# Optimization experiments

Measured on AMD Instinct MI355X. Metric: run time of the kernel, lower is better.

Reference implementation:

```python
import jax, jax.numpy as jnp
import numpy as np

NUM_HEADS = 8  # from init_kwargs
SR = 2         # sr_ratio from init_kwargs


def layernorm(t, g, b, eps=1e-5):
    mu = jnp.mean(t, axis=-1, keepdims=True)
    var = jnp.mean((t - mu) ** 2, axis=-1, keepdims=True)
    return (t - mu) * jax.lax.rsqrt(var + eps) * g + b


def setup_inputs() -> dict:
    key = jax.random.key(0)
    ks = jax.random.split(key, 6)
    B, C = 4, 256
    Hx = Wx = 64
    Hz = Wz = 32
    N = Hz * Wz + Hx * Wx  # 5120 (template tokens first, then search tokens)
    s = 0.02
    return {
        "x": jax.random.normal(ks[0], (B, N, C), jnp.float32),
        "Wq": jax.random.normal(ks[1], (C, C), jnp.float32) * s,          # nn.Linear(dim, dim, bias=False)
        "Wkv": jax.random.normal(ks[2], (2 * C, C), jnp.float32) * s,     # nn.Linear(dim, 2*dim, bias=False)
        "Wsr": jax.random.normal(ks[3], (C, C, SR, SR), jnp.float32) * s, # Conv2d(dim, dim, k=sr, stride=sr) OIHW
        "bsr": jnp.zeros((C,), jnp.float32),
        "gamma": jnp.ones((C,), jnp.float32),
        "beta": jnp.zeros((C,), jnp.float32),
        "Wproj": jax.random.normal(ks[4], (C, C), jnp.float32) * s,
        "bproj": jnp.zeros((C,), jnp.float32),
        "H_x": Hx, "W_x": Wx, "H_z": Hz, "W_z": Wz,
    }


def reference(x, Wq, Wkv, Wsr, bsr, gamma, beta, Wproj, bproj, H_x, W_x, H_z, W_z):
    B, N, C = x.shape
    h = NUM_HEADS
    d = C // h
    scale = d ** -0.5
    Nz, Nx = H_z * W_z, H_x * W_x

    # q for all tokens: [B, h, N, d]
    q = (x @ Wq.T).reshape(B, N, h, d).transpose(0, 2, 1, 3)

    # spatial reduction (sr_ratio > 1 branch): strided conv + layernorm on each stream
    z_tok, x_tok = x[:, :Nz], x[:, Nz:]
    ker = jnp.transpose(Wsr, (2, 3, 1, 0))  # OIHW -> HWIO

    def sr_branch(t, H, W):
        img = t.reshape(B, H, W, C)  # NHWC; same layout as torch NCHW reshape
        out = jax.lax.conv_general_dilated(
            img, ker, window_strides=(SR, SR), padding="VALID",
            dimension_numbers=("NHWC", "HWIO", "NHWC")) + bsr
        out = out.reshape(B, -1, C)
        return layernorm(out, gamma, beta)

    x_ = sr_branch(x_tok, H_x, W_x)  # [B, (Hx/sr)*(Wx/sr), C]
    z_ = sr_branch(z_tok, H_z, W_z)  # [B, (Hz/sr)*(Wz/sr), C]
    zL = z_.shape[1]
    cat = jnp.concatenate([z_, x_], axis=1)  # [B, L, C]

    kv = (cat @ Wkv.T).reshape(B, -1, 2, h, d).transpose(2, 0, 3, 1, 4)  # [2, B, h, L, d]
    k, v = kv[0], kv[1]

    q_z, q_x = q[:, :, :Nz], q[:, :, Nz:]
    k_z, v_z = k[:, :, :zL], v[:, :, :zL]

    # template queries attend only to reduced template keys/values
    attn_z = jax.nn.softmax(jnp.einsum("bhqd,bhkd->bhqk", q_z, k_z) * scale, axis=-1)
    out_z = jnp.einsum("bhqk,bhkd->bhqd", attn_z, v_z).transpose(0, 2, 1, 3).reshape(B, Nz, C)

    # search queries attend to full (template+search) reduced keys/values
    attn_x = jax.nn.softmax(jnp.einsum("bhqd,bhkd->bhqk", q_x, k) * scale, axis=-1)
    out_x = jnp.einsum("bhqk,bhkd->bhqd", attn_x, v).transpose(0, 2, 1, 3).reshape(B, Nx, C)

    out = jnp.concatenate([out_z, out_x], axis=1)
    return out @ Wproj.T + bproj
```

## Files before the change

kernel.cpp:

```cpp
#include <hip/hip_runtime.h>
#include <hip/hip_bf16.h>
#include <cstddef>

#define BATCH 4
#define CCH 256
#define NHEAD 8
#define DHEAD 32
#define NZ 1024
#define NX 4096
#define NTOK 5120
#define LKV 1280
#define QC 0.25503486f

typedef __attribute__((ext_vector_type(8))) short bf16x8;
typedef __attribute__((ext_vector_type(4))) float floatx4;

__device__ inline short f2bf(float f) {
  __hip_bfloat16 h = __float2bfloat16(f);
  return __builtin_bit_cast(short, h);
}
__device__ inline unsigned int pk2(float a, float b) {
  unsigned int lo = (unsigned short)f2bf(a);
  unsigned int hi = (unsigned short)f2bf(b);
  return lo | (hi << 16);
}
__device__ inline unsigned int cvtpk(float a, float b) {
  unsigned int r;
  asm("v_cvt_pk_bf16_f32 %0, %1, %2" : "=v"(r) : "v"(a), "v"(b));
  return r;
}
__device__ inline void cvt8(const float* __restrict__ src, short* __restrict__ dst, int i) {
  float4 v0 = ((const float4*)src)[i * 2];
  float4 v1 = ((const float4*)src)[i * 2 + 1];
  uint4 u;
  u.x = pk2(v0.x, v0.y); u.y = pk2(v0.z, v0.w);
  u.z = pk2(v1.x, v1.y); u.w = pk2(v1.z, v1.w);
  ((uint4*)dst)[i] = u;
}

__global__ __launch_bounds__(256) void prep_weights(const float* __restrict__ Wq,
                                                    const float* __restrict__ Wkv,
                                                    const float* __restrict__ Wproj,
                                                    const float* __restrict__ Wsr,
                                                    const float* __restrict__ x,
                                                    short* __restrict__ Wqb,
                                                    short* __restrict__ Wkvb,
                                                    short* __restrict__ Wprojb,
                                                    short* __restrict__ Wkb,
                                                    short* __restrict__ xb) {
  int blk = blockIdx.x, tid = threadIdx.x;
  if (blk < 32) {
    cvt8(Wq, Wqb, blk * 256 + tid);
  } else if (blk < 96) {
    cvt8(Wkv, Wkvb, (blk - 32) * 256 + tid);
  } else if (blk < 128) {
    cvt8(Wproj, Wprojb, (blk - 96) * 256 + tid);
  } else if (blk < 1152) {
    int i = (blk - 128) * 256 + tid;
    int co = i >> 10;
    int rem = i & 1023;
    int di = rem >> 9, dj = (rem >> 8) & 1, ci = rem & 255;
    Wkb[i] = f2bf(Wsr[((co * 256 + ci) * 2 + di) * 2 + dj]);
  } else {
    cvt8(x, xb, (blk - 1152) * 256 + tid);
  }
}

#define G64_DECL()                                                           \
  __shared__ short As[64][72];                                               \
  __shared__ short Bs[64][72];                                               \
  int tid = threadIdx.x;                                                     \
  int wave = tid >> 6, lg = (tid & 63) >> 4, lr = tid & 15;                  \
  int sr = tid >> 2, sc = tid & 3;                                           \
  floatx4 acc[4] = {{0.f,0.f,0.f,0.f},{0.f,0.f,0.f,0.f},                     \
                    {0.f,0.f,0.f,0.f},{0.f,0.f,0.f,0.f}};

#define G64_MFMA8()                                                          \
    __syncthreads();                                                         \
    {                                                                        \
      bf16x8 af0 = *(bf16x8*)&As[wave * 16 + lr][lg * 8];                    \
      bf16x8 af1 = *(bf16x8*)&As[wave * 16 + lr][32 + lg * 8];               \
      _Pragma("unroll") for (int n = 0; n < 4; ++n) {                        \
        bf16x8 bf0 = *(bf16x8*)&Bs[n * 16 + lr][lg * 8];                     \
        bf16x8 bf1 = *(bf16x8*)&Bs[n * 16 + lr][32 + lg * 8];                \
        acc[n] = __builtin_amdgcn_mfma_f32_16x16x32_bf16(af0, bf0, acc[n], 0, 0, 0); \
        acc[n] = __builtin_amdgcn_mfma_f32_16x16x32_bf16(af1, bf1, acc[n], 0, 0, 0); \
      }                                                                      \
    }

__global__ __launch_bounds__(256) void gemm_qconv(const short* __restrict__ xb,
                                                  const short* __restrict__ Wqb,
                                                  const short* __restrict__ Wkb,
                                                  short* __restrict__ qbf,
                                                  float* __restrict__ cat_pre) {
  G64_DECL()
  int bidx = blockIdx.x;
  if (bidx < 1280) {
    int bm = (bidx >> 2) * 64, bn = (bidx & 3) * 64;
    for (int k0 = 0; k0 < 256; k0 += 64) {
      bf16x8 a0 = *(const bf16x8*)&xb[(size_t)(bm + sr) * 256 + k0 + sc * 8];
      bf16x8 a1 = *(const bf16x8*)&xb[(size_t)(bm + sr) * 256 + k0 + (sc + 4) * 8];
      bf16x8 b0 = *(const bf16x8*)&Wqb[(size_t)(bn + sr) * 256 + k0 + sc * 8];
      bf16x8 b1 = *(const bf16x8*)&Wqb[(size_t)(bn + sr) * 256 + k0 + (sc + 4) * 8];
      __syncthreads();
      *(bf16x8*)&As[sr][sc * 8] = a0;
      *(bf16x8*)&As[sr][(sc + 4) * 8] = a1;
      *(bf16x8*)&Bs[sr][sc * 8] = b0;
      *(bf16x8*)&Bs[sr][(sc + 4) * 8] = b1;
      G64_MFMA8()
    }
#pragma unroll
    for (int n = 0; n < 4; ++n) {
      int c = bn + 16 * n + lr;
      int h = c >> 5, d = c & 31;
#pragma unroll
      for (int reg = 0; reg < 4; ++reg) {
        int m = bm + wave * 16 + 4 * lg + reg;
        int b = m / NTOK, tok = m - b * NTOK;
        qbf[((size_t)(b * 8 + h) * NTOK + tok) * 32 + d] = f2bf(acc[n][reg] * QC);
      }
    }
  } else {
    int idx = bidx - 1280;
    int mt = idx >> 2;
    int bm = mt * 64, bn = (idx & 3) * 64;
    int bq = mt / 20;
    int tloc = (mt % 20) * 64 + sr;
    for (int k0 = 0; k0 < 1024; k0 += 64) {
      int di = k0 >> 9, dj = (k0 >> 8) & 1;
      int srow;
      if (tloc < 256) {
        int oi = tloc >> 4, oj = tloc & 15;
        srow = bq * NTOK + (2 * oi + di) * 32 + (2 * oj + dj);
      } else {
        int tt = tloc - 256;
        int oi = tt >> 5, oj = tt & 31;
        srow = bq * NTOK + NZ + (2 * oi + di) * 64 + (2 * oj + dj);
      }
      int cb = k0 & 255;
      bf16x8 a0 = *(const bf16x8*)&xb[(size_t)srow * 256 + cb + sc * 8];
      bf16x8 a1 = *(const bf16x8*)&xb[(size_t)srow * 256 + cb + (sc + 4) * 8];
      bf16x8 b0 = *(const bf16x8*)&Wkb[(size_t)(bn + sr) * 1024 + k0 + sc * 8];
      bf16x8 b1 = *(const bf16x8*)&Wkb[(size_t)(bn + sr) * 1024 + k0 + (sc + 4) * 8];
      __syncthreads();
      *(bf16x8*)&As[sr][sc * 8] = a0;
      *(bf16x8*)&As[sr][(sc + 4) * 8] = a1;
      *(bf16x8*)&Bs[sr][sc * 8] = b0;
      *(bf16x8*)&Bs[sr][(sc + 4) * 8] = b1;
      G64_MFMA8()
    }
#pragma unroll
    for (int n = 0; n < 4; ++n) {
      int c = bn + 16 * n + lr;
#pragma unroll
      for (int reg = 0; reg < 4; ++reg) {
        int m = bm + wave * 16 + 4 * lg + reg;
        cat_pre[(size_t)m * 256 + c] = acc[n][reg];
      }
    }
  }
}

__global__ __launch_bounds__(256) void gemm_kv64(const short* __restrict__ A,
                                                 const short* __restrict__ Bm,
                                                 short* __restrict__ Kbf,
                                                 short* __restrict__ Vtb) {
  G64_DECL()
  int bm = blockIdx.y * 64, bn = blockIdx.x * 64;
  for (int k0 = 0; k0 < 256; k0 += 64) {
    bf16x8 a0 = *(const bf16x8*)&A[(size_t)(bm + sr) * 256 + k0 + sc * 8];
    bf16x8 a1 = *(const bf16x8*)&A[(size_t)(bm + sr) * 256 + k0 + (sc + 4) * 8];
    bf16x8 b0 = *(const bf16x8*)&Bm[(size_t)(bn + sr) * 256 + k0 + sc * 8];
    bf16x8 b1 = *(const bf16x8*)&Bm[(size_t)(bn + sr) * 256 + k0 + (sc + 4) * 8];
    __syncthreads();
    *(bf16x8*)&As[sr][sc * 8] = a0;
    *(bf16x8*)&As[sr][(sc + 4) * 8] = a1;
    *(bf16x8*)&Bs[sr][sc * 8] = b0;
    *(bf16x8*)&Bs[sr][(sc + 4) * 8] = b1;
    G64_MFMA8()
  }
#pragma unroll
  for (int n = 0; n < 4; ++n) {
    int c = bn + 16 * n + lr;
#pragma unroll
    for (int reg = 0; reg < 4; ++reg) {
      int m = bm + wave * 16 + 4 * lg + reg;
      int b = m / LKV, kvg = m - b * LKV;
      if (c < 256) {
        int h = c >> 5, d = c & 31;
        Kbf[((size_t)(b * 8 + h) * LKV + kvg) * 32 + d] = f2bf(acc[n][reg]);
      } else {
        int cc = c - 256;
        int h = cc >> 5, d = cc & 31;
        int tile = kvg >> 6, kvin = kvg & 63;
        Vtb[(((size_t)(b * 8 + h) * 20 + tile) * 32 + d) * 64 + kvin] = f2bf(acc[n][reg]);
      }
    }
  }
}

__global__ __launch_bounds__(256) void gemm_proj64(const short* __restrict__ A,
                                                   const short* __restrict__ Bm,
                                                   const float* __restrict__ bias,
                                                   float* __restrict__ Cm) {
  G64_DECL()
  int bm = blockIdx.y * 64, bn = blockIdx.x * 64;
  for (int k0 = 0; k0 < 256; k0 += 64) {
    bf16x8 a0 = *(const bf16x8*)&A[(size_t)(bm + sr) * 256 + k0 + sc * 8];
    bf16x8 a1 = *(const bf16x8*)&A[(size_t)(bm + sr) * 256 + k0 + (sc + 4) * 8];
    bf16x8 b0 = *(const bf16x8*)&Bm[(size_t)(bn + sr) * 256 + k0 + sc * 8];
    bf16x8 b1 = *(const bf16x8*)&Bm[(size_t)(bn + sr) * 256 + k0 + (sc + 4) * 8];
    __syncthreads();
    *(bf16x8*)&As[sr][sc * 8] = a0;
    *(bf16x8*)&As[sr][(sc + 4) * 8] = a1;
    *(bf16x8*)&Bs[sr][sc * 8] = b0;
    *(bf16x8*)&Bs[sr][(sc + 4) * 8] = b1;
    G64_MFMA8()
  }
#pragma unroll
  for (int n = 0; n < 4; ++n) {
    int c = bn + 16 * n + lr;
    float bv = bias[c];
#pragma unroll
    for (int reg = 0; reg < 4; ++reg) {
      int m = bm + wave * 16 + 4 * lg + reg;
      Cm[(size_t)m * 256 + c] = acc[n][reg] + bv;
    }
  }
}

__global__ __launch_bounds__(256) void ln_kernel(const float* __restrict__ cat_pre,
                                                 const float* __restrict__ bsr,
                                                 const float* __restrict__ gamma,
                                                 const float* __restrict__ beta,
                                                 short* __restrict__ catb) {
  int row = blockIdx.x * 4 + (threadIdx.x >> 6);
  int lane = threadIdx.x & 63;
  float4 v = *(const float4*)&cat_pre[(size_t)row * 256 + lane * 4];
  float4 bb = *(const float4*)&bsr[lane * 4];
  v.x += bb.x; v.y += bb.y; v.z += bb.z; v.w += bb.w;
  float s = (v.x + v.y) + (v.z + v.w);
#pragma unroll
  for (int mask = 1; mask < 64; mask <<= 1) s += __shfl_xor(s, mask, 64);
  float mu = s * (1.f / 256.f);
  float4 dv;
  dv.x = v.x - mu; dv.y = v.y - mu; dv.z = v.z - mu; dv.w = v.w - mu;
  float q = dv.x * dv.x + dv.y * dv.y + dv.z * dv.z + dv.w * dv.w;
#pragma unroll
  for (int mask = 1; mask < 64; mask <<= 1) q += __shfl_xor(q, mask, 64);
  float rs = rsqrtf(q * (1.f / 256.f) + 1e-5f);
  float4 g = *(const float4*)&gamma[lane * 4];
  float4 be = *(const float4*)&beta[lane * 4];
  uint2 st;
  st.x = pk2(dv.x * rs * g.x + be.x, dv.y * rs * g.y + be.y);
  st.y = pk2(dv.z * rs * g.z + be.z, dv.w * rs * g.w + be.w);
  *(uint2*)&catb[(size_t)row * 256 + lane * 4] = st;
}

__global__ __launch_bounds__(64) void attn_fused(const short* __restrict__ qbf,
                                                 const short* __restrict__ Kbf,
                                                 const short* __restrict__ Vtb,
                                                 short* __restrict__ attn_out) {
  int orig = blockIdx.x;
  int xcd = orig & 7, s = orig >> 3;
  int bh, q0, kvlen;
  if (s < 256) {
    bh = xcd + 8 * (s >> 6);
    q0 = NZ + (s & 63) * 64;
    kvlen = LKV;
  } else {
    int s2 = s - 256;
    bh = xcd + 8 * (s2 >> 4);
    q0 = (s2 & 15) * 64;
    kvlen = 256;
  }
  int b = bh >> 3, hh = bh & 7;
  int tid = threadIdx.x;
  int lane = tid & 63, lg = lane >> 4, lr = lane & 15;

  __shared__ short Ps[64][72];

  int qtok = q0;
  const short* qb = qbf + ((size_t)bh * NTOK + qtok) * 32;
  bf16x8 qf[4];
#pragma unroll
  for (int qi = 0; qi < 4; ++qi)
    qf[qi] = *(const bf16x8*)&qb[(16 * qi + lr) * 32 + lg * 8];

  const short* Kb = Kbf + (size_t)bh * LKV * 32;
  const short* Vb = Vtb + (size_t)bh * 20 * 2048;

  const short onebf = (short)0x3F80;
  bf16x8 onesb = {onebf, onebf, onebf, onebf, onebf, onebf, onebf, onebf};

  floatx4 oacc[4][2];
  floatx4 lacc[4];
#pragma unroll
  for (int qi = 0; qi < 4; ++qi) {
    lacc[qi] = (floatx4){0.f, 0.f, 0.f, 0.f};
#pragma unroll
    for (int n = 0; n < 2; ++n) oacc[qi][n] = (floatx4){0.f, 0.f, 0.f, 0.f};
  }

  bf16x8 kfc[4], vfc[2][2];
#pragma unroll
  for (int m = 0; m < 4; ++m)
    kfc[m] = *(const bf16x8*)&Kb[(size_t)(16 * m + lr) * 32 + lg * 8];
#pragma unroll
  for (int n = 0; n < 2; ++n)
#pragma unroll
    for (int kb = 0; kb < 2; ++kb)
      vfc[n][kb] = *(const bf16x8*)&Vb[(16 * n + lr) * 64 + kb * 32 + lg * 8];

  for (int l0 = 0; l0 < kvlen; l0 += 64) {
    __builtin_amdgcn_sched_barrier(0);
#pragma unroll
    for (int qi = 0; qi < 4; ++qi) {
      floatx4 st[4];
#pragma unroll
      for (int m = 0; m < 4; ++m)
        st[m] = __builtin_amdgcn_mfma_f32_16x16x32_bf16(
            kfc[m], qf[qi], (floatx4){0.f, 0.f, 0.f, 0.f}, 0, 0, 0);
      int pr = 16 * qi + lr;
#pragma unroll
      for (int m = 0; m < 4; ++m) {
        float p0 = __builtin_amdgcn_exp2f(st[m][0]);
        float p1 = __builtin_amdgcn_exp2f(st[m][1]);
        float p2 = __builtin_amdgcn_exp2f(st[m][2]);
        float p3 = __builtin_amdgcn_exp2f(st[m][3]);
        uint2 w;
        w.x = cvtpk(p0, p1);
        w.y = cvtpk(p2, p3);
        *(uint2*)&Ps[pr][16 * m + 4 * lg] = w;
      }
    }

    bf16x8 kfn[4], vfn[2][2];
    int l1 = l0 + 64;
    if (l1 < kvlen) {
      const short* Vbt = Vb + (l1 >> 6) * 2048;
#pragma unroll
      for (int m = 0; m < 4; ++m)
        kfn[m] = *(const bf16x8*)&Kb[(size_t)(l1 + 16 * m + lr) * 32 + lg * 8];
#pragma unroll
      for (int n = 0; n < 2; ++n)
#pragma unroll
        for (int kb = 0; kb < 2; ++kb)
          vfn[n][kb] = *(const bf16x8*)&Vbt[(16 * n + lr) * 64 + kb * 32 + lg * 8];
    }

    __builtin_amdgcn_sched_barrier(0);

#pragma unroll
    for (int qi = 0; qi < 4; ++qi)
#pragma unroll
      for (int kb = 0; kb < 2; ++kb) {
        bf16x8 pf = *(bf16x8*)&Ps[16 * qi + lr][kb * 32 + lg * 8];
#pragma unroll
        for (int n = 0; n < 2; ++n)
          oacc[qi][n] = __builtin_amdgcn_mfma_f32_16x16x32_bf16(pf, vfc[n][kb], oacc[qi][n], 0, 0, 0);
        lacc[qi] = __builtin_amdgcn_mfma_f32_16x16x32_bf16(pf, onesb, lacc[qi], 0, 0, 0);
      }

#pragma unroll
    for (int m = 0; m < 4; ++m) kfc[m] = kfn[m];
#pragma unroll
    for (int n = 0; n < 2; ++n)
#pragma unroll
      for (int kb = 0; kb < 2; ++kb) vfc[n][kb] = vfn[n][kb];
  }

#pragma unroll
  for (int qi = 0; qi < 4; ++qi)
#pragma unroll
    for (int reg = 0; reg < 4; ++reg) {
      float inv = 1.f / lacc[qi][reg];
      int gr = b * NTOK + qtok + 16 * qi + 4 * lg + reg;
      short* ob = attn_out + (size_t)gr * CCH + hh * DHEAD;
      ob[lr]      = f2bf(oacc[qi][0][reg] * inv);
      ob[16 + lr] = f2bf(oacc[qi][1][reg] * inv);
    }
}

extern "C" void kernel_launch(void* const* d_in, const int* in_sizes, int n_in,
                              void* d_out, int out_size, void* d_ws, size_t ws_size,
                              hipStream_t stream) {
  (void)in_sizes; (void)n_in; (void)out_size; (void)ws_size;
  const float* x     = (const float*)d_in[0];
  const float* Wq    = (const float*)d_in[1];
  const float* Wkv   = (const float*)d_in[2];
  const float* Wsr   = (const float*)d_in[3];
  const float* bsr   = (const float*)d_in[4];
  const float* gamma = (const float*)d_in[5];
  const float* beta  = (const float*)d_in[6];
  const float* Wproj = (const float*)d_in[7];
  const float* bproj = (const float*)d_in[8];
  float* out = (float*)d_out;
  float* ws  = (float*)d_ws;

  short* qbf      = (short*)ws;
  short* attn_out = (short*)(ws + 2621440);
  float* cat_pre  = ws + 7864320;
  short* catb     = (short*)(ws + 9175040);
  short* Kbf      = (short*)(ws + 9830400);
  short* Vtb      = (short*)(ws + 10485760);
  short* Wqb      = (short*)(ws + 11141120);
  short* Wkvb     = (short*)(ws + 11173888);
  short* Wkb      = (short*)(ws + 11239424);
  short* Wprojb   = (short*)(ws + 11370496);
  short* xb       = attn_out;

  prep_weights<<<3712, 256, 0, stream>>>(Wq, Wkv, Wproj, Wsr, x, Wqb, Wkvb, Wprojb, Wkb, xb);
  gemm_qconv<<<1600, 256, 0, stream>>>(xb, Wqb, Wkb, qbf, cat_pre);
  ln_kernel<<<1280, 256, 0, stream>>>(cat_pre, bsr, gamma, beta, catb);
  gemm_kv64<<<dim3(8, 80), 256, 0, stream>>>(catb, Wkvb, Kbf, Vtb);
  attn_fused<<<2560, 64, 0, stream>>>(qbf, Kbf, Vtb, attn_out);
  gemm_proj64<<<dim3(4, 320), 256, 0, stream>>>(attn_out, Wprojb, bproj, out);
}
```

Measured before the change: 191.2 us.

## Double-buffer P tiles in attention, compute row sums on VALU, cheaper bf16 pack

Restructures the attention inner loop into a software pipeline with two shared-memory P buffers. The QK^T and exp for tile t+1 now overlap with the PV MFMAs for tile t, and the sched barriers are removed. The row-sum MFMA against a ones vector is replaced by per-lane float accumulation plus shuffle reductions, which cuts MFMA work by a third in the PV phase. The inline cvt_pk bf16 instruction is replaced by a round-half-up bit trick using v_perm. The new pack differs slightly in rounding, and the row sum now uses the unrounded fp32 P, so it no longer matches the bf16 P that feeds the PV MFMAs.

```diff
diff --git a/kernel.cpp b/kernel.cpp
--- a/kernel.cpp
+++ b/kernel.cpp
@@ -24,10 +24,10 @@
   unsigned int hi = (unsigned short)f2bf(b);
   return lo | (hi << 16);
 }
-__device__ inline unsigned int cvtpk(float a, float b) {
-  unsigned int r;
-  asm("v_cvt_pk_bf16_f32 %0, %1, %2" : "=v"(r) : "v"(a), "v"(b));
-  return r;
+__device__ inline unsigned int pk2f(float a, float b) {
+  unsigned int ua = __builtin_bit_cast(unsigned int, a) + 0x8000u;
+  unsigned int ub = __builtin_bit_cast(unsigned int, b) + 0x8000u;
+  return __builtin_amdgcn_perm(ub, ua, 0x07060302u);
 }
 __device__ inline void cvt8(const float* __restrict__ src, short* __restrict__ dst, int i) {
   float4 v0 = ((const float4*)src)[i * 2];
@@ -257,6 +257,45 @@
   *(uint2*)&catb[(size_t)row * 256 + lane * 4] = st;
 }
 
+#define ATTN_HALF(RD, WR, T, LOADK)                                             \
+  {                                                                             \
+    const short* Vbt = Vb + ((T) + 1) * 2048;                                   \
+    _Pragma("unroll") for (int n = 0; n < 2; ++n)                               \
+      _Pragma("unroll") for (int kb = 0; kb < 2; ++kb)                          \
+        vfn[n][kb] = *(const bf16x8*)&Vbt[(16 * n + lr) * 64 + kb * 32 + lg * 8]; \
+    if (LOADK) {                                                                \
+      _Pragma("unroll") for (int m = 0; m < 4; ++m)                             \
+        kfn[m] = *(const bf16x8*)&Kb[(size_t)(((T) + 2) * 64 + 16 * m + lr) * 32 + lg * 8]; \
+    }                                                                           \
+    _Pragma("unroll") for (int qi = 0; qi < 4; ++qi) {                          \
+      floatx4 st[4];                                                            \
+      _Pragma("unroll") for (int m = 0; m < 4; ++m)                             \
+        st[m] = __builtin_amdgcn_mfma_f32_16x16x32_bf16(                        \
+            kfc[m], qf[qi], (floatx4){0.f, 0.f, 0.f, 0.f}, 0, 0, 0);            \
+      int pr = 16 * qi + lr;                                                    \
+      _Pragma("unroll") for (int m = 0; m < 4; ++m) {                           \
+        float p0 = __builtin_amdgcn_exp2f(st[m][0]);                            \
+        float p1 = __builtin_amdgcn_exp2f(st[m][1]);                            \
+        float p2 = __builtin_amdgcn_exp2f(st[m][2]);                            \
+        float p3 = __builtin_amdgcn_exp2f(st[m][3]);                            \
+        lsum[qi] += (p0 + p1) + (p2 + p3);                                      \
+        uint2 w;                                                                \
+        w.x = pk2f(p0, p1);                                                     \
+        w.y = pk2f(p2, p3);                                                     \
+        *(uint2*)&WR[pr][16 * m + 4 * lg] = w;                                  \
+      }                                                                         \
+    }                                                                           \
+    _Pragma("unroll") for (int qi = 0; qi < 4; ++qi)                            \
+      _Pragma("unroll") for (int kb = 0; kb < 2; ++kb) {                        \
+        bf16x8 pf = *(bf16x8*)&RD[16 * qi + lr][kb * 32 + lg * 8];              \
+        _Pragma("unroll") for (int n = 0; n < 2; ++n)                           \
+          oacc[qi][n] = __builtin_amdgcn_mfma_f32_16x16x32_bf16(pf, vfc[n][kb], oacc[qi][n], 0, 0, 0); \
+      }                                                                         \
+    _Pragma("unroll") for (int m = 0; m < 4; ++m) kfc[m] = kfn[m];              \
+    _Pragma("unroll") for (int n = 0; n < 2; ++n)                               \
+      _Pragma("unroll") for (int kb = 0; kb < 2; ++kb) vfc[n][kb] = vfn[n][kb]; \
+  }
+
 __global__ __launch_bounds__(64) void attn_fused(const short* __restrict__ qbf,
                                                  const short* __restrict__ Kbf,
                                                  const short* __restrict__ Vtb,
@@ -278,7 +317,8 @@
   int tid = threadIdx.x;
   int lane = tid & 63, lg = lane >> 4, lr = lane & 15;
 
-  __shared__ short Ps[64][72];
+  __shared__ short PsA[64][72];
+  __shared__ short PsB[64][72];
 
   int qtok = q0;
   const short* qb = qbf + ((size_t)bh * NTOK + qtok) * 32;
@@ -290,19 +330,16 @@
   const short* Kb = Kbf + (size_t)bh * LKV * 32;
   const short* Vb = Vtb + (size_t)bh * 20 * 2048;
 
-  const short onebf = (short)0x3F80;
-  bf16x8 onesb = {onebf, onebf, onebf, onebf, onebf, onebf, onebf, onebf};
-
   floatx4 oacc[4][2];
-  floatx4 lacc[4];
-#pragma unroll
-  for (int qi = 0; qi < 4; ++qi) {
-    lacc[qi] = (floatx4){0.f, 0.f, 0.f, 0.f};
+#pragma unroll
+  for (int qi = 0; qi < 4; ++qi)
 #pragma unroll
     for (int n = 0; n < 2; ++n) oacc[qi][n] = (floatx4){0.f, 0.f, 0.f, 0.f};
-  }
-
-  bf16x8 kfc[4], vfc[2][2];
+  float lsum[4] = {0.f, 0.f, 0.f, 0.f};
+
+  int nt = kvlen >> 6;
+
+  bf16x8 kfc[4], vfc[2][2], kfn[4], vfn[2][2];
 #pragma unroll
   for (int m = 0; m < 4; ++m)
     kfc[m] = *(const bf16x8*)&Kb[(size_t)(16 * m + lr) * 32 + lg * 8];
@@ -312,69 +349,59 @@
     for (int kb = 0; kb < 2; ++kb)
       vfc[n][kb] = *(const bf16x8*)&Vb[(16 * n + lr) * 64 + kb * 32 + lg * 8];
 
-  for (int l0 = 0; l0 < kvlen; l0 += 64) {
-    __builtin_amdgcn_sched_barrier(0);
-#pragma unroll
-    for (int qi = 0; qi < 4; ++qi) {
-      floatx4 st[4];
-#pragma unroll
-      for (int m = 0; m < 4; ++m)
-        st[m] = __builtin_amdgcn_mfma_f32_16x16x32_bf16(
-            kfc[m], qf[qi], (floatx4){0.f, 0.f, 0.f, 0.f}, 0, 0, 0);
-      int pr = 16 * qi + lr;
-#pragma unroll
-      for (int m = 0; m < 4; ++m) {
-        float p0 = __builtin_amdgcn_exp2f(st[m][0]);
-        float p1 = __builtin_amdgcn_exp2f(st[m][1]);
-        float p2 = __builtin_amdgcn_exp2f(st[m][2]);
-        float p3 = __builtin_amdgcn_exp2f(st[m][3]);
-        uint2 w;
-        w.x = cvtpk(p0, p1);
-        w.y = cvtpk(p2, p3);
-        *(uint2*)&Ps[pr][16 * m + 4 * lg] = w;
-      }
-    }
-
-    bf16x8 kfn[4], vfn[2][2];
-    int l1 = l0 + 64;
-    if (l1 < kvlen) {
-      const short* Vbt = Vb + (l1 >> 6) * 2048;
-#pragma unroll
-      for (int m = 0; m < 4; ++m)
-        kfn[m] = *(const bf16x8*)&Kb[(size_t)(l1 + 16 * m + lr) * 32 + lg * 8];
+#pragma unroll
+  for (int qi = 0; qi < 4; ++qi) {
+    floatx4 st[4];
+#pragma unroll
+    for (int m = 0; m < 4; ++m)
+      st[m] = __builtin_amdgcn_mfma_f32_16x16x32_bf16(
+          kfc[m], qf[qi], (floatx4){0.f, 0.f, 0.f, 0.f}, 0, 0, 0);
+    int pr = 16 * qi + lr;
+#pragma unroll
+    for (int m = 0; m < 4; ++m) {
+      float p0 = __builtin_amdgcn_exp2f(st[m][0]);
+      float p1 = __builtin_amdgcn_exp2f(st[m][1]);
+      float p2 = __builtin_amdgcn_exp2f(st[m][2]);
+      float p3 = __builtin_amdgcn_exp2f(st[m][3]);
+      lsum[qi] += (p0 + p1) + (p2 + p3);
+      uint2 w;
+      w.x = pk2f(p0, p1);
+      w.y = pk2f(p2, p3);
+      *(uint2*)&PsA[pr][16 * m + 4 * lg] = w;
+    }
+  }
+#pragma unroll
+  for (int m = 0; m < 4; ++m)
+    kfc[m] = *(const bf16x8*)&Kb[(size_t)(64 + 16 * m + lr) * 32 + lg * 8];
+
+  for (int t = 0; t < nt - 2; t += 2) {
+    ATTN_HALF(PsA, PsB, t, 1)
+    ATTN_HALF(PsB, PsA, t + 1, 1)
+  }
+  ATTN_HALF(PsA, PsB, nt - 2, 0)
+
+#pragma unroll
+  for (int qi = 0; qi < 4; ++qi)
+#pragma unroll
+    for (int kb = 0; kb < 2; ++kb) {
+      bf16x8 pf = *(bf16x8*)&PsB[16 * qi + lr][kb * 32 + lg * 8];
 #pragma unroll
       for (int n = 0; n < 2; ++n)
-#pragma unroll
-        for (int kb = 0; kb < 2; ++kb)
-          vfn[n][kb] = *(const bf16x8*)&Vbt[(16 * n + lr) * 64 + kb * 32 + lg * 8];
-    }
-
-    __builtin_amdgcn_sched_barrier(0);
-
-#pragma unroll
-    for (int qi = 0; qi < 4; ++qi)
-#pragma unroll
-      for (int kb = 0; kb < 2; ++kb) {
-        bf16x8 pf = *(bf16x8*)&Ps[16 * qi + lr][kb * 32 + lg * 8];
-#pragma unroll
-        for (int n = 0; n < 2; ++n)
-          oacc[qi][n] = __builtin_amdgcn_mfma_f32_16x16x32_bf16(pf, vfc[n][kb], oacc[qi][n], 0, 0, 0);
-        lacc[qi] = __builtin_amdgcn_mfma_f32_16x16x32_bf16(pf, onesb, lacc[qi], 0, 0, 0);
-      }
-
-#pragma unroll
-    for (int m = 0; m < 4; ++m) kfc[m] = kfn[m];
-#pragma unroll
-    for (int n = 0; n < 2; ++n)
-#pragma unroll
-      for (int kb = 0; kb < 2; ++kb) vfc[n][kb] = vfn[n][kb];
+        oacc[qi][n] = __builtin_amdgcn_mfma_f32_16x16x32_bf16(pf, vfc[n][kb], oacc[qi][n], 0, 0, 0);
+    }
+
+#pragma unroll
+  for (int qi = 0; qi < 4; ++qi) {
+    lsum[qi] += __shfl_xor(lsum[qi], 16, 64);
+    lsum[qi] += __shfl_xor(lsum[qi], 32, 64);
   }
 
 #pragma unroll
   for (int qi = 0; qi < 4; ++qi)
 #pragma unroll
     for (int reg = 0; reg < 4; ++reg) {
-      float inv = 1.f / lacc[qi][reg];
+      float lv = __shfl(lsum[qi], 4 * lg + reg, 64);
+      float inv = 1.f / lv;
       int gr = b * NTOK + qtok + 16 * qi + 4 * lg + reg;
       short* ob = attn_out + (size_t)gr * CCH + hh * DHEAD;
       ob[lr]      = f2bf(oacc[qi][0][reg] * inv);
```

Result: faster. 184.8 us (-3.4%).
